# Optimization experiments

Hardware: AMD Instinct MI355X
Metric: run time of the kernel (lower is better)

The kernel has to match this reference:

```python
import jax, jax.numpy as jnp
import numpy as np
import math

D_MODEL = 512
NHEAD = 8
D_K = D_MODEL // NHEAD
MIN_WL, MAX_WL, BASE, EPS = 3.7, 20.0, 20.0, 0.02


def setup_inputs() -> dict:
    key = jax.random.key(0)
    ks = jax.random.split(key, 9)
    B, N = 2, 2048
    q = jax.random.normal(ks[0], (B, N, D_MODEL), dtype=jnp.float32)
    k = jax.random.normal(ks[1], (B, N, D_MODEL), dtype=jnp.float32)
    v = jax.random.normal(ks[2], (B, N, D_MODEL), dtype=jnp.float32)
    # scale coords so pairwise distances fall in the 3.7-20 Angstrom regime
    coords = jax.random.normal(ks[3], (B, N, 3), dtype=jnp.float32) * 10.0
    key_padding_mask = jnp.zeros((B, N), dtype=bool)
    q_proj = jax.random.normal(ks[4], (NHEAD, D_MODEL, D_K), dtype=jnp.float32)
    k_proj = jax.random.normal(ks[5], (NHEAD, D_MODEL, D_K), dtype=jnp.float32)
    v_proj = jax.random.normal(ks[6], (NHEAD, D_MODEL, D_K), dtype=jnp.float32)
    out_w = jax.random.normal(ks[7], (D_MODEL, D_MODEL), dtype=jnp.float32) / math.sqrt(D_MODEL)
    out_b = jax.random.normal(ks[8], (D_MODEL,), dtype=jnp.float32) * 0.01
    return {"q": q, "k": k, "v": v, "coords": coords,
            "key_padding_mask": key_padding_mask,
            "q_proj": q_proj, "k_proj": k_proj, "v_proj": v_proj,
            "out_w": out_w, "out_b": out_b}


def _spreads():
    # torch.logspace(0, 1-eps, nhead, base) == base ** linspace(0, 1-eps, nhead)
    log = BASE ** jnp.linspace(0.0, 1.0 - EPS, NHEAD, dtype=jnp.float32)
    return MIN_WL + (log - 1.0) / (BASE - 1.0) * (MAX_WL - MIN_WL)  # [H]


def reference(q, k, v, coords, key_padding_mask, q_proj, k_proj, v_proj, out_w, out_b):
    B, N, _ = q.shape
    # per-head projections: [B,H,N,d_k]
    qh = jnp.einsum('bnd,hdk->bhnk', q, q_proj)
    kh = jnp.einsum('bnd,hdk->bhnk', k, k_proj)
    vh = jnp.einsum('bnd,hdk->bhnk', v, v_proj)
    attn = jnp.einsum('bhqk,bhmk->bhqm', qh, kh) / math.sqrt(D_K)  # [B,H,N,N]

    # pairwise distances [B,1,N,N], head spreads [1,H,1,1]
    diff = coords[:, None, :, :] - coords[:, :, None, :]
    dists = jnp.sqrt(jnp.sum(diff * diff, axis=-1))[:, None, :, :]
    spreads = _spreads()[None, :, None, None]

    # clamp: dists < spread -> spread; dists > 3*spread -> 3*spread (and masked)
    dists = jnp.maximum(dists, spreads)                 # [B,H,N,N]
    dist_mask = dists > 3.0 * spreads
    dists = jnp.minimum(dists, 3.0 * spreads)

    rbf = jnp.exp(-(dists * dists) / (2.0 * spreads * spreads))
    rbf = jnp.where(attn < 0, 1.0 / rbf, rbf)
    attn = attn * rbf

    attn_mask = key_padding_mask[:, None, None, :] | dist_mask
    attn = jnp.where(attn_mask, -jnp.inf, attn)
    attn = jax.nn.softmax(attn, axis=-1)

    out = jnp.einsum('bhqm,bhmk->bhqk', attn, vh)       # [B,H,N,d_k]
    out = out.transpose(0, 2, 1, 3).reshape(B, N, D_MODEL)
    return out @ out_w.T + out_b
```

## Files before the change

kernel.cpp:

```cpp
#include <hip/hip_runtime.h>
#include <hip/hip_bf16.h>

typedef unsigned short u16;
typedef __attribute__((ext_vector_type(8))) short bf16x8;
typedef __attribute__((ext_vector_type(8))) unsigned short u16x8;
typedef __attribute__((ext_vector_type(4))) unsigned short u16x4;
typedef __attribute__((ext_vector_type(4))) float f32x4;

#define B_ 2
#define H_ 8
#define N_ 2048
#define DK_ 64
#define DM_ 512

#define NEG_BIG (-1.0e30f)

__device__ __forceinline__ float bf2f(u16 u){
  union { unsigned int i; float f; } x; x.i = ((unsigned int)u) << 16; return x.f;
}
__device__ __forceinline__ u16 f2bf(float f){
  union { float f; unsigned int i; } x; x.f = f;
  unsigned int r = x.i + 0x7fffu + ((x.i >> 16) & 1u);
  return (u16)(r >> 16);
}

__global__ void k_tpose(const float* __restrict__ qp, const float* __restrict__ kp,
                        const float* __restrict__ vp,
                        u16* __restrict__ wq_hi, u16* __restrict__ wq_lo,
                        u16* __restrict__ wk_hi, u16* __restrict__ wk_lo,
                        u16* __restrict__ wv_hi, u16* __restrict__ wv_lo){
  int idx = blockIdx.x * 256 + threadIdx.x;
  int d = idx & 511, c = idx >> 9;
  int h = c >> 6, kk = c & 63;
  int z = blockIdx.y;
  const float* s = (z == 0) ? qp : (z == 1) ? kp : vp;
  u16* thi = (z == 0) ? wq_hi : (z == 1) ? wk_hi : wv_hi;
  u16* tlo = (z == 0) ? wq_lo : (z == 1) ? wk_lo : wv_lo;
  float x = s[h * (512 * 64) + d * 64 + kk];
  u16 hi = f2bf(x);
  thi[c * 512 + d] = hi;
  tlo[c * 512 + d] = f2bf(x - bf2f(hi));
}

__global__ void k_coordsT(const float* __restrict__ coords,
                          float* __restrict__ cx, float* __restrict__ cy,
                          float* __restrict__ cz){
  int idx = blockIdx.x * 256 + threadIdx.x;
  cx[idx] = coords[idx * 3];
  cy[idx] = coords[idx * 3 + 1];
  cz[idx] = coords[idx * 3 + 2];
}

__global__ void k_split(const float* __restrict__ q, const float* __restrict__ k,
                        const float* __restrict__ v,
                        u16* __restrict__ qAhi, u16* __restrict__ qAlo,
                        u16* __restrict__ kAhi, u16* __restrict__ kAlo,
                        u16* __restrict__ vAhi, u16* __restrict__ vAlo){
  int z = blockIdx.y;
  const float* src = (z == 0) ? q : (z == 1) ? k : v;
  u16* dhi = (z == 0) ? qAhi : (z == 1) ? kAhi : vAhi;
  u16* dlo = (z == 0) ? qAlo : (z == 1) ? kAlo : vAlo;
  int i = (blockIdx.x * 256 + threadIdx.x) * 8;
  float4 f0 = *(const float4*)&src[i];
  float4 f1 = *(const float4*)&src[i + 4];
  float xs[8] = {f0.x, f0.y, f0.z, f0.w, f1.x, f1.y, f1.z, f1.w};
  u16x8 th, tl;
#pragma unroll
  for (int j = 0; j < 8; j++) {
    u16 hi = f2bf(xs[j]);
    th[j] = hi;
    tl[j] = f2bf(xs[j] - bf2f(hi));
  }
  *(u16x8*)&dhi[i] = th;
  *(u16x8*)&dlo[i] = tl;
}

__global__ void k_wconv(const float* __restrict__ ow, u16* __restrict__ wbf){
  int i = (blockIdx.x * 256 + threadIdx.x) * 4;
  float4 f = *(const float4*)&ow[i];
  u16x4 t;
  t[0] = f2bf(f.x); t[1] = f2bf(f.y); t[2] = f2bf(f.z); t[3] = f2bf(f.w);
  *(u16x4*)&wbf[i] = t;
}

__global__ __launch_bounds__(256) void k_proj(
    const u16* __restrict__ qAhi, const u16* __restrict__ qAlo,
    const u16* __restrict__ kAhi, const u16* __restrict__ kAlo,
    const u16* __restrict__ vAhi, const u16* __restrict__ vAlo,
    const u16* __restrict__ wq_hi, const u16* __restrict__ wq_lo,
    const u16* __restrict__ wk_hi, const u16* __restrict__ wk_lo,
    const u16* __restrict__ wv_hi, const u16* __restrict__ wv_lo,
    u16* __restrict__ qh_hi, u16* __restrict__ qh_lo,
    u16* __restrict__ kh_hi, u16* __restrict__ kh_lo, u16* __restrict__ vt)
{
  int z = blockIdx.z;
  const u16* Ahi = (z == 0) ? qAhi : (z == 1) ? kAhi : vAhi;
  const u16* Alo = (z == 0) ? qAlo : (z == 1) ? kAlo : vAlo;
  const u16* Whi = (z == 0) ? wq_hi : (z == 1) ? wk_hi : wv_hi;
  const u16* Wlo = (z == 0) ? wq_lo : (z == 1) ? wk_lo : wv_lo;
  __shared__ u16 AsH[64 * 40], AsL[64 * 40], BsH[64 * 40], BsL[64 * 40];
  int tid = threadIdx.x, w = tid >> 6, l = tid & 63, quad = l >> 4, n16 = l & 15;
  int m0 = blockIdx.x * 64, c0 = blockIdx.y * 64;
  int srow = tid >> 2, sc = (tid & 3) * 8;
  f32x4 acc[4] = {{0,0,0,0},{0,0,0,0},{0,0,0,0},{0,0,0,0}};
  for (int k0 = 0; k0 < 512; k0 += 32) {
    *(float4*)&AsH[srow * 40 + sc] = *(const float4*)&Ahi[(m0 + srow) * 512 + k0 + sc];
    *(float4*)&AsL[srow * 40 + sc] = *(const float4*)&Alo[(m0 + srow) * 512 + k0 + sc];
    *(float4*)&BsH[srow * 40 + sc] = *(const float4*)&Whi[(c0 + srow) * 512 + k0 + sc];
    *(float4*)&BsL[srow * 40 + sc] = *(const float4*)&Wlo[(c0 + srow) * 512 + k0 + sc];
    __syncthreads();
    bf16x8 ah = *(bf16x8*)&AsH[(w * 16 + n16) * 40 + quad * 8];
    bf16x8 al = *(bf16x8*)&AsL[(w * 16 + n16) * 40 + quad * 8];
#pragma unroll
    for (int ct = 0; ct < 4; ct++) {
      bf16x8 bh = *(bf16x8*)&BsH[(ct * 16 + n16) * 40 + quad * 8];
      bf16x8 bl = *(bf16x8*)&BsL[(ct * 16 + n16) * 40 + quad * 8];
      acc[ct] = __builtin_amdgcn_mfma_f32_16x16x32_bf16(ah, bh, acc[ct], 0, 0, 0);
      acc[ct] = __builtin_amdgcn_mfma_f32_16x16x32_bf16(ah, bl, acc[ct], 0, 0, 0);
      acc[ct] = __builtin_amdgcn_mfma_f32_16x16x32_bf16(al, bh, acc[ct], 0, 0, 0);
    }
    __syncthreads();
  }
#pragma unroll
  for (int ct = 0; ct < 4; ct++) {
#pragma unroll
    for (int reg = 0; reg < 4; reg++) {
      float val = acc[ct][reg];
      int m = m0 + w * 16 + quad * 4 + reg;
      int c = c0 + ct * 16 + n16;
      int b = m >> 11, n = m & 2047;
      int h = c >> 6, kk = c & 63;
      if (z == 2) {
        vt[((b * 8 + h) * 64 + kk) * 2048 + n] = f2bf(val);
      } else {
        int di = ((b * 8 + h) * 2048 + n) * 64 + kk;
        u16 hib = f2bf(val);
        u16 lob = f2bf(val - bf2f(hib));
        if (z == 0) { qh_hi[di] = hib; qh_lo[di] = lob; }
        else        { kh_hi[di] = hib; kh_lo[di] = lob; }
      }
    }
  }
}

__global__ __launch_bounds__(256, 4) void k_attn(
    const u16* __restrict__ qh_hi, const u16* __restrict__ qh_lo,
    const u16* __restrict__ kh_hi, const u16* __restrict__ kh_lo,
    const u16* __restrict__ vt,
    const float* __restrict__ cx, const float* __restrict__ cy,
    const float* __restrict__ cz,
    float* __restrict__ pO, float* __restrict__ pM, float* __restrict__ pL)
{
  int q0 = blockIdx.x * 64;
  int bh = blockIdx.y; int b = bh >> 3, h = bh & 7;
  int half = blockIdx.z;
  int tid = threadIdx.x, w = tid >> 6, l = tid & 63, quad = l >> 4, n16 = l & 15;

  double t = 0.98 * (double)h / 7.0;
  float s = (float)(3.7 + (pow(20.0, t) - 1.0) / 19.0 * 16.3);
  float s2 = s * s;
  float nine_s2 = 9.0f * s2;
  float inv2s2 = 1.0f / (2.0f * s2);

  __shared__ u16 Khi[64 * 72], Klo[64 * 72], Vt[64 * 72];
  __shared__ float kcx[64], kcy[64], kcz[64];
  __shared__ u16 Plds[4][16 * 72];

  int qrow = q0 + w * 16 + n16;
  const u16* qb  = qh_hi + ((size_t)bh * 2048 + qrow) * 64 + quad * 8;
  const u16* qbl = qh_lo + ((size_t)bh * 2048 + qrow) * 64 + quad * 8;
  bf16x8 qfh0 = *(const bf16x8*)qb;
  bf16x8 qfh1 = *(const bf16x8*)(qb + 32);
  bf16x8 qfl0 = *(const bf16x8*)qbl;
  bf16x8 qfl1 = *(const bf16x8*)(qbl + 32);

  float qx[4], qy[4], qz[4];
#pragma unroll
  for (int reg = 0; reg < 4; reg++) {
    int r = b * 2048 + q0 + w * 16 + quad * 4 + reg;
    qx[reg] = cx[r]; qy[reg] = cy[r]; qz[reg] = cz[r];
  }

  float mrow[4], lrow[4];
  f32x4 oacc[4] = {{0,0,0,0},{0,0,0,0},{0,0,0,0},{0,0,0,0}};
#pragma unroll
  for (int reg = 0; reg < 4; reg++) { mrow[reg] = NEG_BIG; lrow[reg] = 0.0f; }

  for (int tt = 0; tt < 16; tt++) {
    int k0 = half * 1024 + tt * 64;

#pragma unroll
    for (int it = 0; it < 2; it++) {
      int cid = tid + it * 256;
      int row = cid >> 3, part = cid & 7;
      *(float4*)&Khi[row * 72 + part * 8] = *(const float4*)&kh_hi[((size_t)bh * 2048 + k0 + row) * 64 + part * 8];
      *(float4*)&Klo[row * 72 + part * 8] = *(const float4*)&kh_lo[((size_t)bh * 2048 + k0 + row) * 64 + part * 8];
      *(float4*)&Vt [row * 72 + part * 8] = *(const float4*)&vt  [((size_t)bh * 64 + row) * 2048 + k0 + part * 8];
    }
    if (tid < 64) {
      int g = b * 2048 + k0 + tid;
      kcx[tid] = cx[g]; kcy[tid] = cy[g]; kcz[tid] = cz[g];
    }
    __syncthreads();

    f32x4 sacc[4] = {{0,0,0,0},{0,0,0,0},{0,0,0,0},{0,0,0,0}};
#pragma unroll
    for (int ct = 0; ct < 4; ct++) {
      int rb = (ct * 16 + n16) * 72;
      bf16x8 kh0 = *(bf16x8*)&Khi[rb + quad * 8];
      bf16x8 kh1 = *(bf16x8*)&Khi[rb + 32 + quad * 8];
      bf16x8 kl0 = *(bf16x8*)&Klo[rb + quad * 8];
      bf16x8 kl1 = *(bf16x8*)&Klo[rb + 32 + quad * 8];
      sacc[ct] = __builtin_amdgcn_mfma_f32_16x16x32_bf16(qfh0, kh0, sacc[ct], 0, 0, 0);
      sacc[ct] = __builtin_amdgcn_mfma_f32_16x16x32_bf16(qfl0, kh0, sacc[ct], 0, 0, 0);
      sacc[ct] = __builtin_amdgcn_mfma_f32_16x16x32_bf16(qfh0, kl0, sacc[ct], 0, 0, 0);
      sacc[ct] = __builtin_amdgcn_mfma_f32_16x16x32_bf16(qfh1, kh1, sacc[ct], 0, 0, 0);
      sacc[ct] = __builtin_amdgcn_mfma_f32_16x16x32_bf16(qfl1, kh1, sacc[ct], 0, 0, 0);
      sacc[ct] = __builtin_amdgcn_mfma_f32_16x16x32_bf16(qfh1, kl1, sacc[ct], 0, 0, 0);
    }

    float lgv[4][4];
#pragma unroll
    for (int ct = 0; ct < 4; ct++) {
      int kl_ = ct * 16 + n16;
      float kx = kcx[kl_], ky = kcy[kl_], kz = kcz[kl_];
#pragma unroll
      for (int reg = 0; reg < 4; reg++) {
        float dx = qx[reg] - kx, dy = qy[reg] - ky, dz = qz[reg] - kz;
        float d2 = dx * dx + dy * dy + dz * dz;
        float attnv = sacc[ct][reg] * 0.125f;
        float d2c = fminf(fmaxf(d2, s2), nine_s2);
        float arg = d2c * inv2s2;
        float lg = attnv * __expf(attnv < 0.0f ? arg : -arg);
        lgv[ct][reg] = (d2 > nine_s2) ? NEG_BIG : lg;
      }
    }

    float pv[4][4];
#pragma unroll
    for (int reg = 0; reg < 4; reg++) {
      float mx = fmaxf(fmaxf(lgv[0][reg], lgv[1][reg]), fmaxf(lgv[2][reg], lgv[3][reg]));
#pragma unroll
      for (int off = 1; off < 16; off <<= 1) mx = fmaxf(mx, __shfl_xor(mx, off));
      float mnew = fmaxf(mrow[reg], mx);
      float alpha = __expf(fminf(mrow[reg] - mnew, 0.0f));
      mrow[reg] = mnew;
      lrow[reg] *= alpha;
      float rs = 0.0f;
#pragma unroll
      for (int ct = 0; ct < 4; ct++) {
        float pp = (lgv[ct][reg] > -1.0e29f)
                 ? __expf(fminf(lgv[ct][reg] - mnew, 0.0f)) : 0.0f;
        pv[ct][reg] = pp;
        rs += pp;
      }
#pragma unroll
      for (int off = 1; off < 16; off <<= 1) rs += __shfl_xor(rs, off);
      lrow[reg] += rs;
#pragma unroll
      for (int ct = 0; ct < 4; ct++) oacc[ct][reg] *= alpha;
    }

#pragma unroll
    for (int ct = 0; ct < 4; ct++)
#pragma unroll
      for (int reg = 0; reg < 4; reg++)
        Plds[w][(quad * 4 + reg) * 72 + ct * 16 + n16] = f2bf(pv[ct][reg]);

    bf16x8 pf0 = *(bf16x8*)&Plds[w][n16 * 72 + quad * 8];
    bf16x8 pf1 = *(bf16x8*)&Plds[w][n16 * 72 + 32 + quad * 8];
#pragma unroll
    for (int ct = 0; ct < 4; ct++) {
      int rb = (ct * 16 + n16) * 72;
      bf16x8 vf0 = *(bf16x8*)&Vt[rb + quad * 8];
      bf16x8 vf1 = *(bf16x8*)&Vt[rb + 32 + quad * 8];
      oacc[ct] = __builtin_amdgcn_mfma_f32_16x16x32_bf16(pf0, vf0, oacc[ct], 0, 0, 0);
      oacc[ct] = __builtin_amdgcn_mfma_f32_16x16x32_bf16(pf1, vf1, oacc[ct], 0, 0, 0);
    }
    __syncthreads();
  }

  size_t rbase = (size_t)(half * 16 + bh) * 2048;
#pragma unroll
  for (int reg = 0; reg < 4; reg++) {
    int row = q0 + w * 16 + quad * 4 + reg;
    if (n16 == 0) { pM[rbase + row] = mrow[reg]; pL[rbase + row] = lrow[reg]; }
#pragma unroll
    for (int ct = 0; ct < 4; ct++)
      pO[(rbase + row) * 64 + ct * 16 + n16] = oacc[ct][reg];
  }
}

__global__ __launch_bounds__(256) void k_merge(
    const float* __restrict__ pO, const float* __restrict__ pM,
    const float* __restrict__ pL, u16* __restrict__ attn_out)
{
  int gid = blockIdx.x * 256 + threadIdx.x;
  int rowId = gid >> 4;
  int c4 = (gid & 15) * 4;
  float m0 = pM[rowId], m1 = pM[32768 + rowId];
  float l0 = pL[rowId], l1 = pL[32768 + rowId];
  float mg = fmaxf(m0, m1);
  float e0 = __expf(fminf(m0 - mg, 0.0f));
  float e1 = __expf(fminf(m1 - mg, 0.0f));
  float inv = 1.0f / fmaxf(l0 * e0 + l1 * e1, 1e-30f);
  float4 o0 = *(const float4*)&pO[(size_t)rowId * 64 + c4];
  float4 o1 = *(const float4*)&pO[(size_t)(32768 + rowId) * 64 + c4];
  int bh = rowId >> 11, row = rowId & 2047, b = bh >> 3, h = bh & 7;
  u16x4 tb;
  tb[0] = f2bf((o0.x * e0 + o1.x * e1) * inv);
  tb[1] = f2bf((o0.y * e0 + o1.y * e1) * inv);
  tb[2] = f2bf((o0.z * e0 + o1.z * e1) * inv);
  tb[3] = f2bf((o0.w * e0 + o1.w * e1) * inv);
  *(u16x4*)&attn_out[((size_t)b * 2048 + row) * 512 + h * 64 + c4] = tb;
}

__global__ __launch_bounds__(256) void k_outp(
    const u16* __restrict__ A, const u16* __restrict__ Wb,
    const float* __restrict__ bias, float* __restrict__ out)
{
  __shared__ u16 As[64 * 40], Bs[64 * 40];
  int tid = threadIdx.x, w = tid >> 6, l = tid & 63, quad = l >> 4, n16 = l & 15;
  int m0 = blockIdx.x * 64, c0 = blockIdx.y * 64;
  int srow = tid >> 2, sc = (tid & 3) * 8;
  f32x4 acc[4] = {{0,0,0,0},{0,0,0,0},{0,0,0,0},{0,0,0,0}};
  for (int k0 = 0; k0 < 512; k0 += 32) {
    *(float4*)&As[srow * 40 + sc] = *(const float4*)&A [(m0 + srow) * 512 + k0 + sc];
    *(float4*)&Bs[srow * 40 + sc] = *(const float4*)&Wb[(c0 + srow) * 512 + k0 + sc];
    __syncthreads();
    bf16x8 af = *(bf16x8*)&As[(w * 16 + n16) * 40 + quad * 8];
#pragma unroll
    for (int ct = 0; ct < 4; ct++) {
      bf16x8 bfr = *(bf16x8*)&Bs[(ct * 16 + n16) * 40 + quad * 8];
      acc[ct] = __builtin_amdgcn_mfma_f32_16x16x32_bf16(af, bfr, acc[ct], 0, 0, 0);
    }
    __syncthreads();
  }
#pragma unroll
  for (int ct = 0; ct < 4; ct++) {
#pragma unroll
    for (int reg = 0; reg < 4; reg++) {
      int m = m0 + w * 16 + quad * 4 + reg;
      int c = c0 + ct * 16 + n16;
      out[m * 512 + c] = acc[ct][reg] + bias[c];
    }
  }
}

extern "C" void kernel_launch(void* const* d_in, const int* in_sizes, int n_in,
                              void* d_out, int out_size, void* d_ws, size_t ws_size,
                              hipStream_t stream)
{
  const float* q      = (const float*)d_in[0];
  const float* k      = (const float*)d_in[1];
  const float* v      = (const float*)d_in[2];
  const float* coords = (const float*)d_in[3];
  const float* qp = (const float*)d_in[5];
  const float* kp = (const float*)d_in[6];
  const float* vp = (const float*)d_in[7];
  const float* ow = (const float*)d_in[8];
  const float* ob = (const float*)d_in[9];
  float* out = (float*)d_out;

  const size_t ACT = (size_t)4096 * 512 * 2;
  char* base = (char*)d_ws;
  u16* qAhi = (u16*)(base);
  u16* qAlo = (u16*)(base + ACT);
  u16* kAhi = (u16*)(base + 2 * ACT);
  u16* kAlo = (u16*)(base + 3 * ACT);
  u16* vAhi = (u16*)(base + 4 * ACT);
  u16* vAlo = (u16*)(base + 5 * ACT);
  float* pO = (float*)(base);
  char* p = base + 6 * ACT;
  auto carve = [&](size_t bytes) -> char* {
    char* r = p; p += (bytes + 255) & ~(size_t)255; return r;
  };
  u16* wq_hi = (u16*)carve((size_t)512 * 512 * 2);
  u16* wq_lo = (u16*)carve((size_t)512 * 512 * 2);
  u16* wk_hi = (u16*)carve((size_t)512 * 512 * 2);
  u16* wk_lo = (u16*)carve((size_t)512 * 512 * 2);
  u16* wv_hi = (u16*)carve((size_t)512 * 512 * 2);
  u16* wv_lo = (u16*)carve((size_t)512 * 512 * 2);
  u16* wbf   = (u16*)carve((size_t)512 * 512 * 2);
  u16* qh_hi = (u16*)carve((size_t)B_ * H_ * N_ * DK_ * 2);
  u16* qh_lo = (u16*)carve((size_t)B_ * H_ * N_ * DK_ * 2);
  u16* kh_hi = (u16*)carve((size_t)B_ * H_ * N_ * DK_ * 2);
  u16* kh_lo = (u16*)carve((size_t)B_ * H_ * N_ * DK_ * 2);
  u16* vt    = (u16*)carve((size_t)B_ * H_ * N_ * DK_ * 2);
  u16* attn_o= (u16*)carve((size_t)B_ * N_ * DM_ * 2);
  float* pM  = (float*)carve((size_t)2 * 16 * 2048 * 4);
  float* pL  = (float*)carve((size_t)2 * 16 * 2048 * 4);
  float* cx  = (float*)carve((size_t)B_ * N_ * 4);
  float* cy  = (float*)carve((size_t)B_ * N_ * 4);
  float* cz  = (float*)carve((size_t)B_ * N_ * 4);

  hipLaunchKernelGGL(k_tpose, dim3(1024, 3), dim3(256), 0, stream,
                     qp, kp, vp, wq_hi, wq_lo, wk_hi, wk_lo, wv_hi, wv_lo);
  hipLaunchKernelGGL(k_coordsT, dim3(16), dim3(256), 0, stream,
                     coords, cx, cy, cz);
  hipLaunchKernelGGL(k_split, dim3(1024, 3), dim3(256), 0, stream,
                     q, k, v, qAhi, qAlo, kAhi, kAlo, vAhi, vAlo);
  hipLaunchKernelGGL(k_wconv, dim3(256), dim3(256), 0, stream, ow, wbf);
  hipLaunchKernelGGL(k_proj, dim3(64, 8, 3), dim3(256), 0, stream,
                     qAhi, qAlo, kAhi, kAlo, vAhi, vAlo,
                     wq_hi, wq_lo, wk_hi, wk_lo, wv_hi, wv_lo,
                     qh_hi, qh_lo, kh_hi, kh_lo, vt);
  hipLaunchKernelGGL(k_attn, dim3(32, 16, 2), dim3(256), 0, stream,
                     qh_hi, qh_lo, kh_hi, kh_lo, vt, cx, cy, cz, pO, pM, pL);
  hipLaunchKernelGGL(k_merge, dim3(2048), dim3(256), 0, stream,
                     pO, pM, pL, attn_o);
  hipLaunchKernelGGL(k_outp, dim3(64, 8), dim3(256), 0, stream,
                     attn_o, wbf, ob, out);
}
```

Baseline: 259.8 us.

## Compute pairwise squared distances via MFMA using split-bf16 augmented coordinate vectors

Rewrites squared distance as |q|^2 + |k|^2 - 2 q·k and packs augmented hi/lo bf16 coordinate vectors per point, so each 16x16 distance tile comes from one MFMA instead of per-element scalar FMAs. It also folds the output-weight conversion into the transpose kernel to drop a launch, and splits the P staging through LDS into two halves to shrink shared memory. The expansion form may lose precision through cancellation near the clamp thresholds, and key geometry is now read straight from global memory inside the loop.

Result: faster. 243.9 us (-6.1%).

```diff
diff --git a/kernel.cpp b/kernel.cpp
--- a/kernel.cpp
+++ b/kernel.cpp
@@ -28,11 +28,22 @@
                         const float* __restrict__ vp,
                         u16* __restrict__ wq_hi, u16* __restrict__ wq_lo,
                         u16* __restrict__ wk_hi, u16* __restrict__ wk_lo,
-                        u16* __restrict__ wv_hi, u16* __restrict__ wv_lo){
+                        u16* __restrict__ wv_hi, u16* __restrict__ wv_lo,
+                        const float* __restrict__ ow, u16* __restrict__ wbf){
+  int z = blockIdx.y;
+  if (z == 3) {
+    if (blockIdx.x < 256) {
+      int i = (blockIdx.x * 256 + threadIdx.x) * 4;
+      float4 f = *(const float4*)&ow[i];
+      u16x4 t;
+      t[0] = f2bf(f.x); t[1] = f2bf(f.y); t[2] = f2bf(f.z); t[3] = f2bf(f.w);
+      *(u16x4*)&wbf[i] = t;
+    }
+    return;
+  }
   int idx = blockIdx.x * 256 + threadIdx.x;
   int d = idx & 511, c = idx >> 9;
   int h = c >> 6, kk = c & 63;
-  int z = blockIdx.y;
   const float* s = (z == 0) ? qp : (z == 1) ? kp : vp;
   u16* thi = (z == 0) ? wq_hi : (z == 1) ? wk_hi : wv_hi;
   u16* tlo = (z == 0) ? wq_lo : (z == 1) ? wk_lo : wv_lo;
@@ -42,13 +53,33 @@
   tlo[c * 512 + d] = f2bf(x - bf2f(hi));
 }
 
-__global__ void k_coordsT(const float* __restrict__ coords,
-                          float* __restrict__ cx, float* __restrict__ cy,
-                          float* __restrict__ cz){
-  int idx = blockIdx.x * 256 + threadIdx.x;
-  cx[idx] = coords[idx * 3];
-  cy[idx] = coords[idx * 3 + 1];
-  cz[idx] = coords[idx * 3 + 2];
+__global__ void k_geom(const float* __restrict__ coords,
+                       u16* __restrict__ Qg, u16* __restrict__ Kg){
+  int n = blockIdx.x * 256 + threadIdx.x;
+  float x = coords[n * 3], y = coords[n * 3 + 1], z = coords[n * 3 + 2];
+  float sq = x * x + y * y + z * z;
+  float tx = -2.0f * x, ty = -2.0f * y, tz = -2.0f * z;
+  u16 xh = f2bf(x);   u16 xl = f2bf(x - bf2f(xh));
+  u16 yh = f2bf(y);   u16 yl = f2bf(y - bf2f(yh));
+  u16 zh = f2bf(z);   u16 zl = f2bf(z - bf2f(zh));
+  u16 txh = f2bf(tx); u16 txl = f2bf(tx - bf2f(txh));
+  u16 tyh = f2bf(ty); u16 tyl = f2bf(ty - bf2f(tyh));
+  u16 tzh = f2bf(tz); u16 tzl = f2bf(tz - bf2f(tzh));
+  u16 sqh = f2bf(sq); u16 sql = f2bf(sq - bf2f(sqh));
+  const u16 ONE = 0x3F80;
+  u16x8 zer = {0,0,0,0,0,0,0,0};
+  u16x8 q0 = {txh, txh, txl, tyh, tyh, tyl, tzh, tzh};
+  u16x8 q1 = {tzl, sqh, sql, ONE, ONE, 0, 0, 0};
+  *(u16x8*)&Qg[n * 32]      = q0;
+  *(u16x8*)&Qg[n * 32 + 8]  = q1;
+  *(u16x8*)&Qg[n * 32 + 16] = zer;
+  *(u16x8*)&Qg[n * 32 + 24] = zer;
+  u16x8 k0 = {xh, xl, xh, yh, yl, yh, zh, zl};
+  u16x8 k1 = {zh, ONE, ONE, sqh, sql, 0, 0, 0};
+  *(u16x8*)&Kg[n * 32]      = k0;
+  *(u16x8*)&Kg[n * 32 + 8]  = k1;
+  *(u16x8*)&Kg[n * 32 + 16] = zer;
+  *(u16x8*)&Kg[n * 32 + 24] = zer;
 }
 
 __global__ void k_split(const float* __restrict__ q, const float* __restrict__ k,
@@ -73,14 +104,6 @@
   }
   *(u16x8*)&dhi[i] = th;
   *(u16x8*)&dlo[i] = tl;
-}
-
-__global__ void k_wconv(const float* __restrict__ ow, u16* __restrict__ wbf){
-  int i = (blockIdx.x * 256 + threadIdx.x) * 4;
-  float4 f = *(const float4*)&ow[i];
-  u16x4 t;
-  t[0] = f2bf(f.x); t[1] = f2bf(f.y); t[2] = f2bf(f.z); t[3] = f2bf(f.w);
-  *(u16x4*)&wbf[i] = t;
 }
 
 __global__ __launch_bounds__(256) void k_proj(
@@ -147,8 +170,7 @@
     const u16* __restrict__ qh_hi, const u16* __restrict__ qh_lo,
     const u16* __restrict__ kh_hi, const u16* __restrict__ kh_lo,
     const u16* __restrict__ vt,
-    const float* __restrict__ cx, const float* __restrict__ cy,
-    const float* __restrict__ cz,
+    const u16* __restrict__ Qg, const u16* __restrict__ Kg,
     float* __restrict__ pO, float* __restrict__ pM, float* __restrict__ pL)
 {
   int q0 = blockIdx.x * 64;
@@ -163,8 +185,7 @@
   float inv2s2 = 1.0f / (2.0f * s2);
 
   __shared__ u16 Khi[64 * 72], Klo[64 * 72], Vt[64 * 72];
-  __shared__ float kcx[64], kcy[64], kcz[64];
-  __shared__ u16 Plds[4][16 * 72];
+  __shared__ u16 Plds[4][16 * 40];
 
   int qrow = q0 + w * 16 + n16;
   const u16* qb  = qh_hi + ((size_t)bh * 2048 + qrow) * 64 + quad * 8;
@@ -173,13 +194,7 @@
   bf16x8 qfh1 = *(const bf16x8*)(qb + 32);
   bf16x8 qfl0 = *(const bf16x8*)qbl;
   bf16x8 qfl1 = *(const bf16x8*)(qbl + 32);
-
-  float qx[4], qy[4], qz[4];
-#pragma unroll
-  for (int reg = 0; reg < 4; reg++) {
-    int r = b * 2048 + q0 + w * 16 + quad * 4 + reg;
-    qx[reg] = cx[r]; qy[reg] = cy[r]; qz[reg] = cz[r];
-  }
+  bf16x8 qg = *(const bf16x8*)&Qg[((size_t)(b * 2048) + qrow) * 32 + quad * 8];
 
   float mrow[4], lrow[4];
   f32x4 oacc[4] = {{0,0,0,0},{0,0,0,0},{0,0,0,0},{0,0,0,0}};
@@ -197,15 +212,15 @@
       *(float4*)&Klo[row * 72 + part * 8] = *(const float4*)&kh_lo[((size_t)bh * 2048 + k0 + row) * 64 + part * 8];
       *(float4*)&Vt [row * 72 + part * 8] = *(const float4*)&vt  [((size_t)bh * 64 + row) * 2048 + k0 + part * 8];
     }
-    if (tid < 64) {
-      int g = b * 2048 + k0 + tid;
-      kcx[tid] = cx[g]; kcy[tid] = cy[g]; kcz[tid] = cz[g];
-    }
     __syncthreads();
 
     f32x4 sacc[4] = {{0,0,0,0},{0,0,0,0},{0,0,0,0},{0,0,0,0}};
-#pragma unroll
-    for (int ct = 0; ct < 4; ct++) {
+    f32x4 dacc[4];
+#pragma unroll
+    for (int ct = 0; ct < 4; ct++) {
+      bf16x8 kg = *(const bf16x8*)&Kg[((size_t)(b * 2048 + k0 + ct * 16 + n16)) * 32 + quad * 8];
+      f32x4 dz = {0,0,0,0};
+      dacc[ct] = __builtin_amdgcn_mfma_f32_16x16x32_bf16(qg, kg, dz, 0, 0, 0);
       int rb = (ct * 16 + n16) * 72;
       bf16x8 kh0 = *(bf16x8*)&Khi[rb + quad * 8];
       bf16x8 kh1 = *(bf16x8*)&Khi[rb + 32 + quad * 8];
@@ -222,12 +237,9 @@
     float lgv[4][4];
 #pragma unroll
     for (int ct = 0; ct < 4; ct++) {
-      int kl_ = ct * 16 + n16;
-      float kx = kcx[kl_], ky = kcy[kl_], kz = kcz[kl_];
 #pragma unroll
       for (int reg = 0; reg < 4; reg++) {
-        float dx = qx[reg] - kx, dy = qy[reg] - ky, dz = qz[reg] - kz;
-        float d2 = dx * dx + dy * dy + dz * dz;
+        float d2 = dacc[ct][reg];
         float attnv = sacc[ct][reg] * 0.125f;
         float d2c = fminf(fmaxf(d2, s2), nine_s2);
         float arg = d2c * inv2s2;
@@ -262,19 +274,25 @@
     }
 
 #pragma unroll
-    for (int ct = 0; ct < 4; ct++)
+    for (int cc = 0; cc < 2; cc++)
 #pragma unroll
       for (int reg = 0; reg < 4; reg++)
-        Plds[w][(quad * 4 + reg) * 72 + ct * 16 + n16] = f2bf(pv[ct][reg]);
-
-    bf16x8 pf0 = *(bf16x8*)&Plds[w][n16 * 72 + quad * 8];
-    bf16x8 pf1 = *(bf16x8*)&Plds[w][n16 * 72 + 32 + quad * 8];
-#pragma unroll
-    for (int ct = 0; ct < 4; ct++) {
-      int rb = (ct * 16 + n16) * 72;
-      bf16x8 vf0 = *(bf16x8*)&Vt[rb + quad * 8];
-      bf16x8 vf1 = *(bf16x8*)&Vt[rb + 32 + quad * 8];
+        Plds[w][(quad * 4 + reg) * 40 + cc * 16 + n16] = f2bf(pv[cc][reg]);
+    bf16x8 pf0 = *(bf16x8*)&Plds[w][n16 * 40 + quad * 8];
+#pragma unroll
+    for (int ct = 0; ct < 4; ct++) {
+      bf16x8 vf0 = *(bf16x8*)&Vt[(ct * 16 + n16) * 72 + quad * 8];
       oacc[ct] = __builtin_amdgcn_mfma_f32_16x16x32_bf16(pf0, vf0, oacc[ct], 0, 0, 0);
+    }
+#pragma unroll
+    for (int cc = 2; cc < 4; cc++)
+#pragma unroll
+      for (int reg = 0; reg < 4; reg++)
+        Plds[w][(quad * 4 + reg) * 40 + (cc - 2) * 16 + n16] = f2bf(pv[cc][reg]);
+    bf16x8 pf1 = *(bf16x8*)&Plds[w][n16 * 40 + quad * 8];
+#pragma unroll
+    for (int ct = 0; ct < 4; ct++) {
+      bf16x8 vf1 = *(bf16x8*)&Vt[(ct * 16 + n16) * 72 + 32 + quad * 8];
       oacc[ct] = __builtin_amdgcn_mfma_f32_16x16x32_bf16(pf1, vf1, oacc[ct], 0, 0, 0);
     }
     __syncthreads();
@@ -390,23 +408,20 @@
   u16* attn_o= (u16*)carve((size_t)B_ * N_ * DM_ * 2);
   float* pM  = (float*)carve((size_t)2 * 16 * 2048 * 4);
   float* pL  = (float*)carve((size_t)2 * 16 * 2048 * 4);
-  float* cx  = (float*)carve((size_t)B_ * N_ * 4);
-  float* cy  = (float*)carve((size_t)B_ * N_ * 4);
-  float* cz  = (float*)carve((size_t)B_ * N_ * 4);
-
-  hipLaunchKernelGGL(k_tpose, dim3(1024, 3), dim3(256), 0, stream,
-                     qp, kp, vp, wq_hi, wq_lo, wk_hi, wk_lo, wv_hi, wv_lo);
-  hipLaunchKernelGGL(k_coordsT, dim3(16), dim3(256), 0, stream,
-                     coords, cx, cy, cz);
+  u16* Qg    = (u16*)carve((size_t)B_ * N_ * 32 * 2);
+  u16* Kgg   = (u16*)carve((size_t)B_ * N_ * 32 * 2);
+
+  hipLaunchKernelGGL(k_tpose, dim3(1024, 4), dim3(256), 0, stream,
+                     qp, kp, vp, wq_hi, wq_lo, wk_hi, wk_lo, wv_hi, wv_lo, ow, wbf);
+  hipLaunchKernelGGL(k_geom, dim3(16), dim3(256), 0, stream, coords, Qg, Kgg);
   hipLaunchKernelGGL(k_split, dim3(1024, 3), dim3(256), 0, stream,
                      q, k, v, qAhi, qAlo, kAhi, kAlo, vAhi, vAlo);
-  hipLaunchKernelGGL(k_wconv, dim3(256), dim3(256), 0, stream, ow, wbf);
   hipLaunchKernelGGL(k_proj, dim3(64, 8, 3), dim3(256), 0, stream,
                      qAhi, qAlo, kAhi, kAlo, vAhi, vAlo,
                      wq_hi, wq_lo, wk_hi, wk_lo, wv_hi, wv_lo,
                      qh_hi, qh_lo, kh_hi, kh_lo, vt);
   hipLaunchKernelGGL(k_attn, dim3(32, 16, 2), dim3(256), 0, stream,
-                     qh_hi, qh_lo, kh_hi, kh_lo, vt, cx, cy, cz, pO, pM, pL);
+                     qh_hi, qh_lo, kh_hi, kh_lo, vt, Qg, Kgg, pO, pM, pL);
   hipLaunchKernelGGL(k_merge, dim3(2048), dim3(256), 0, stream,
                      pO, pM, pL, attn_o);
   hipLaunchKernelGGL(k_outp, dim3(64, 8), dim3(256), 0, stream,
```
